# Kernel tuning notes

Hardware: AMD Instinct MI355X
Metric: run time of the kernel (lower is better)

Reference implementation:

```python
import jax, jax.numpy as jnp
import numpy as np

D = 64        # gat_output_dim == state_dim
HID = 128     # hidden_dim
ADIM = 2 * D  # action_dim (ope_dim + insert_dim)


def _mk(key, shape, scale=0.05):
    return jax.random.normal(key, shape, dtype=jnp.float32) * scale


def setup_inputs() -> dict:
    key = jax.random.key(0)
    ks = jax.random.split(key, 24)
    inp = {
        "ope_gat": jax.random.normal(ks[0], (8, 258, D), jnp.float32),
        "insert_gat": jax.random.normal(ks[1], (8, 256, D), jnp.float32),
        "h": jax.random.normal(ks[2], (8, D), jnp.float32),
        "c": jax.random.normal(ks[3], (8, D), jnp.float32),
        # LSTM (pytorch layout: gates i,f,g,o stacked -> [4D, in])
        "W_ih": _mk(ks[4], (4 * D, D)),
        "W_hh": _mk(ks[5], (4 * D, D)),
        "b_ih": _mk(ks[6], (4 * D,)),
        "b_hh": _mk(ks[7], (4 * D,)),
        # V_net: Linear(D,HID) -> Linear(HID,HID) -> LeakyReLU -> Linear(HID,1)
        "Wv0": _mk(ks[8], (HID, D)), "bv0": _mk(ks[9], (HID,)),
        "Wv1": _mk(ks[10], (HID, HID)), "bv1": _mk(ks[11], (HID,)),
        "Wv2": _mk(ks[12], (1, HID)), "bv2": _mk(ks[13], (1,)),
        # A_net: Linear(D+ADIM,HID) -> Linear(HID,HID) -> LeakyReLU -> Linear(HID,1)
        "Wa0": _mk(ks[14], (HID, D + ADIM)), "ba0": _mk(ks[15], (HID,)),
        "Wa1": _mk(ks[16], (HID, HID)), "ba1": _mk(ks[17], (HID,)),
        "Wa2": _mk(ks[18], (1, HID)), "ba2": _mk(ks[19], (1,)),
    }
    return inp


def _lrelu(x):
    return jnp.where(x >= 0, x, 0.01 * x)


def _forward(ope_gat, insert_gat, h, c,
             W_ih, W_hh, b_ih, b_hh,
             Wv0, bv0, Wv1, bv1, Wv2, bv2,
             Wa0, ba0, Wa1, ba1, Wa2, ba2):
    ope = ope_gat[:, 1:-1]                # [B, O, D]
    state = ope.mean(axis=-2)             # [B, D]

    # single-step LSTM (pytorch gate order i, f, g, o)
    gates = state @ W_ih.T + b_ih + h @ W_hh.T + b_hh  # [B, 4D]
    i_g, f_g, g_g, o_g = jnp.split(gates, 4, axis=-1)
    cn = jax.nn.sigmoid(f_g) * c + jax.nn.sigmoid(i_g) * jnp.tanh(g_g)
    hn = jax.nn.sigmoid(o_g) * jnp.tanh(cn)
    rnn_state = hn                        # [B, D]

    # V head (note: no activation after first linear -- name-overwrite bug)
    V = _lrelu((rnn_state @ Wv0.T + bv0) @ Wv1.T + bv1) @ Wv2.T + bv2  # [B, 1]

    # A head on the full (ope x insert) cross-join; ope side is detached.
    ope_d = jax.lax.stop_gradient(ope)    # [B, O, D]
    B, O, _ = ope_d.shape
    I = insert_gat.shape[1]
    # Decompose first linear over the concat [state | ope | insert] (exact math).
    Ws, Wo, Wi = Wa0[:, :D], Wa0[:, D:2 * D], Wa0[:, 2 * D:]
    h0 = (rnn_state @ Ws.T)[:, None, None, :] \
         + jnp.einsum('bod,hd->boh', ope_d, Wo)[:, :, None, :] \
         + jnp.einsum('bid,hd->bih', insert_gat, Wi)[:, None, :, :] \
         + ba0                              # [B, O, I, HID]
    h1 = _lrelu(jnp.einsum('boih,gh->boig', h0, Wa1) + ba1)
    A = (jnp.einsum('boih,h->boi', h1, Wa2[0]) + ba2[0]).reshape(B, O * I)
    return V, A, hn, cn


def reference(ope_gat, insert_gat, h, c,
              W_ih, W_hh, b_ih, b_hh,
              Wv0, bv0, Wv1, bv1, Wv2, bv2,
              Wa0, ba0, Wa1, ba1, Wa2, ba2):
    return _forward(ope_gat, insert_gat, h, c,
                    W_ih, W_hh, b_ih, b_hh,
                    Wv0, bv0, Wv1, bv1, Wv2, bv2,
                    Wa0, ba0, Wa1, ba1, Wa2, ba2)
```

## Files before the change

kernel.cpp:

```cpp
#include <hip/hip_runtime.h>
#include <hip/hip_bf16.h>
#include <math.h>

typedef unsigned short u16;

#define FB    524288
#define PART  6416
#define WA1B  10512
#define WOB   18704
#define WIB   22800
#define SOFF  26896
#define C1S   27920

__device__ __forceinline__ u16 f2b(float x) { __hip_bfloat16 b = __float2bfloat16(x); return *(u16*)&b; }
__device__ __forceinline__ void cvt8(const uint4 u, float* f) {
    f[0] = __uint_as_float(u.x << 16); f[1] = __uint_as_float(u.x & 0xFFFF0000u);
    f[2] = __uint_as_float(u.y << 16); f[3] = __uint_as_float(u.y & 0xFFFF0000u);
    f[4] = __uint_as_float(u.z << 16); f[5] = __uint_as_float(u.z & 0xFFFF0000u);
    f[6] = __uint_as_float(u.w << 16); f[7] = __uint_as_float(u.w & 0xFFFF0000u);
}
__device__ __forceinline__ float dot4(const float4 a, const float4 b) {
    return a.x*b.x + a.y*b.y + a.z*b.z + a.w*b.w;
}

__global__ __launch_bounds__(256) void k0_pre(
    const float* __restrict__ ope, const float* __restrict__ Wa0,
    const float* __restrict__ Wa1, const float* __restrict__ Wa2,
    const float* __restrict__ ba2, float* __restrict__ ws)
{
    const int t = threadIdx.x;
    if (blockIdx.x < 64) {
        const int b = blockIdx.x >> 3, s = blockIdx.x & 7;
        const int d = t & 63, rg = t >> 6;
        __shared__ float red[256];
        const float* p = ope + b*16512 + (1 + s*32 + rg*8)*64 + d;
        float acc = 0.f;
        #pragma unroll
        for (int rr = 0; rr < 8; ++rr) acc += p[rr*64];
        red[t] = acc;
        __syncthreads();
        if (t < 64)
            ws[FB + PART + (b*8 + s)*64 + t] = red[t] + red[t+64] + red[t+128] + red[t+192];
    } else if (blockIdx.x < 80) {
        const int e0 = ((blockIdx.x - 64)*256 + t) * 8;
        const float* src;
        u16* dst;
        if (e0 < 16384)      { src = Wa1 + e0;                                              dst = (u16*)(ws + FB + WA1B) + e0; }
        else if (e0 < 24576) { const int i = e0 - 16384; src = Wa0 + (i>>6)*192 + 64  + (i&63); dst = (u16*)(ws + FB + WOB) + i; }
        else                 { const int i = e0 - 24576; src = Wa0 + (i>>6)*192 + 128 + (i&63); dst = (u16*)(ws + FB + WIB) + i; }
        const float4 a = *(const float4*)src;
        const float4 c = *(const float4*)(src + 4);
        ushort4 u0; u0.x = f2b(a.x); u0.y = f2b(a.y); u0.z = f2b(a.z); u0.w = f2b(a.w);
        ushort4 u1; u1.x = f2b(c.x); u1.y = f2b(c.y); u1.z = f2b(c.z); u1.w = f2b(c.w);
        *(ushort4*)dst = u0;
        *(ushort4*)(dst + 4) = u1;
    } else {
        if (t < 128) {
            const float w2v = Wa2[t];
            ws[FB + 1024 + t] = 0.505f * w2v;
            ws[FB + 1152 + t] = 0.495f * w2v;
        }
        if (t == 128) ws[FB + 2313] = ba2[0];
    }
}

__global__ __launch_bounds__(256) void k12_main(
    const float* __restrict__ ope, const float* __restrict__ ins,
    const float* __restrict__ hin, const float* __restrict__ cin,
    const float* __restrict__ W_ih, const float* __restrict__ W_hh,
    const float* __restrict__ b_ih, const float* __restrict__ b_hh,
    const float* __restrict__ Wv0, const float* __restrict__ bv0,
    const float* __restrict__ Wv1, const float* __restrict__ bv1,
    const float* __restrict__ Wv2, const float* __restrict__ bv2,
    const float* __restrict__ Wa0, const float* __restrict__ ba0,
    const float* __restrict__ Wa1, const float* __restrict__ ba1,
    float* __restrict__ ws)
{
    __shared__ __align__(16) u16 Wa1s[128*136];
    __shared__ __align__(16) u16 Wsel[128*72];
    __shared__ __align__(16) u16 inrows[16*72];
    __shared__ __align__(16) float P[16*132];
    const int t = threadIdx.x;

    if (blockIdx.x < 256) {
        const int b = blockIdx.x >> 5;
        const int r0 = (blockIdx.x & 31) * 16;
        const int side = (r0 >= 256) ? 1 : 0;

        {
            const u16* wa1b = (const u16*)(ws + FB + WA1B);
            #pragma unroll
            for (int k = 0; k < 8; ++k) {
                const int e4 = t + k*256;
                const int g = e4 >> 4, hq = (e4 & 15) * 8;
                *(uint4*)&Wa1s[g*136 + hq] = *(const uint4*)(wa1b + g*128 + hq);
            }
        }
        {
            const u16* wsb = (const u16*)(ws + FB + (side ? WIB : WOB));
            #pragma unroll
            for (int k = 0; k < 4; ++k) {
                const int e4 = t + k*256;
                const int h = e4 >> 3, dq = (e4 & 7) * 8;
                *(uint4*)&Wsel[h*72 + dq] = *(const uint4*)(wsb + h*64 + dq);
            }
        }
        {
            const int r = t >> 4, dq = (t & 15) * 4;
            const float* src = side
                ? (ins + b*16384 + (r0 - 256 + r)*64 + dq)
                : (ope + b*16512 + (1 + r0 + r)*64 + dq);
            const float4 w = *(const float4*)src;
            ushort4 u; u.x = f2b(w.x); u.y = f2b(w.y); u.z = f2b(w.z); u.w = f2b(w.w);
            *(ushort4*)&inrows[r*72 + dq] = u;
        }
        __syncthreads();

        const int r = t >> 4;
        const int q = t & 15;

        {
            float acc[8] = {0.f,0.f,0.f,0.f,0.f,0.f,0.f,0.f};
            #pragma unroll
            for (int d8 = 0; d8 < 64; d8 += 8) {
                float iv[8];
                cvt8(*(const uint4*)&inrows[r*72 + d8], iv);
                #pragma unroll
                for (int k = 0; k < 8; ++k) {
                    float wv[8];
                    cvt8(*(const uint4*)&Wsel[(q + 16*k)*72 + d8], wv);
                    #pragma unroll
                    for (int j = 0; j < 8; ++j) acc[k] += wv[j] * iv[j];
                }
            }
            #pragma unroll
            for (int k = 0; k < 8; ++k) P[r*132 + q + 16*k] = acc[k];
        }
        __syncthreads();

        {
            float acc[8] = {0.f,0.f,0.f,0.f,0.f,0.f,0.f,0.f};
            #pragma unroll
            for (int h8 = 0; h8 < 128; h8 += 8) {
                const float4 p0 = *(const float4*)&P[r*132 + h8];
                const float4 p1 = *(const float4*)&P[r*132 + h8 + 4];
                #pragma unroll
                for (int k = 0; k < 8; ++k) {
                    float wv[8];
                    cvt8(*(const uint4*)&Wa1s[(q + 16*k)*136 + h8], wv);
                    float a = acc[k];
                    a += wv[0]*p0.x + wv[1]*p0.y + wv[2]*p0.z + wv[3]*p0.w;
                    a += wv[4]*p1.x + wv[5]*p1.y + wv[6]*p1.z + wv[7]*p1.w;
                    acc[k] = a;
                }
            }
            float part = 0.f;
            const int row = side ? (b*256 + r0 - 256 + r) : (b*256 + r0 + r);
            float* dst = side ? (ws + 262144 + row*128) : (ws + row*128);
            #pragma unroll
            for (int k = 0; k < 8; ++k) {
                const int g = q + 16*k;
                part = fmaf(ws[FB + 1024 + g], acc[k], part);
                dst[g] = acc[k];
            }
            part += __shfl_xor(part, 1);
            part += __shfl_xor(part, 2);
            part += __shfl_xor(part, 4);
            part += __shfl_xor(part, 8);
            if (q == 0) {
                if (!side) ws[FB + 2320 + row] = part;
                else       ws[FB + 4368 + row] = part;
            }
        }
    } else {
        const int b = blockIdx.x - 256;
        float* f = (float*)Wa1s;
        float* state = f;
        float* hvec  = f + 64;
        float* gl    = f + 128;
        float* hn_s  = f + 384;
        float* t0a   = f + 448;
        float* t1a   = f + 576;
        float* s2s   = f + 704;
        float* red   = f + 832;

        if (t < 64) {
            float s = 0.f;
            #pragma unroll
            for (int s8 = 0; s8 < 8; ++s8) s += ws[FB + PART + (b*8 + s8)*64 + t];
            state[t] = s * (1.f/256.f);
        } else if (t < 128) hvec[t-64] = hin[b*64 + (t-64)];
        __syncthreads();

        {
            float g = b_ih[t] + b_hh[t];
            const float4* wi = (const float4*)(W_ih + t*64);
            const float4* wh = (const float4*)(W_hh + t*64);
            #pragma unroll
            for (int k = 0; k < 16; ++k)
                g += dot4(wi[k], *(const float4*)&state[k*4])
                   + dot4(wh[k], *(const float4*)&hvec[k*4]);
            gl[t] = g;
        }
        __syncthreads();

        if (t < 64) {
            const float ig = gl[t], fg = gl[64+t], gg = gl[128+t], og = gl[192+t];
            const float c  = cin[b*64 + t];
            const float si = 1.f/(1.f + expf(-ig));
            const float sf = 1.f/(1.f + expf(-fg));
            const float so = 1.f/(1.f + expf(-og));
            const float cn = sf*c + si*tanhf(gg);
            const float hn = so*tanhf(cn);
            ws[FB + 1288 + b*64 + t] = hn;
            ws[FB + 1800 + b*64 + t] = cn;
            hn_s[t] = hn;
        }
        __syncthreads();

        if (t < 128) {
            float a = bv0[t];
            const float4* w = (const float4*)(Wv0 + t*64);
            #pragma unroll
            for (int k = 0; k < 16; ++k) a += dot4(w[k], *(const float4*)&hn_s[k*4]);
            t0a[t] = a;
        }
        __syncthreads();
        if (t < 128) {
            float a = bv1[t];
            const float4* w = (const float4*)(Wv1 + t*128);
            #pragma unroll
            for (int k = 0; k < 32; ++k) a += dot4(w[k], *(const float4*)&t0a[k*4]);
            a = (a >= 0.f) ? a : 0.01f*a;
            t1a[t] = a * Wv2[t];
            float s2 = ba0[t];
            const float4* w0 = (const float4*)(Wa0 + t*192);
            #pragma unroll
            for (int k = 0; k < 16; ++k) s2 += dot4(w0[k], *(const float4*)&hn_s[k*4]);
            s2s[t] = s2;
        }
        __syncthreads();
        if (t < 128) {
            float sv = ba1[t];
            const float4* w = (const float4*)(Wa1 + t*128);
            #pragma unroll
            for (int k = 0; k < 32; ++k) sv += dot4(w[k], *(const float4*)&s2s[k*4]);
            ws[FB + SOFF + b*128 + t] = sv;
            red[t] = ws[FB + 1024 + t] * sv;
        }
        __syncthreads();
        if (t < 64) {
            float c = red[t] + red[t + 64];
            float v = t1a[t] + t1a[t + 64];
            c += __shfl_xor(c, 32); v += __shfl_xor(v, 32);
            c += __shfl_xor(c, 16); v += __shfl_xor(v, 16);
            c += __shfl_xor(c, 8);  v += __shfl_xor(v, 8);
            c += __shfl_xor(c, 4);  v += __shfl_xor(v, 4);
            c += __shfl_xor(c, 2);  v += __shfl_xor(v, 2);
            c += __shfl_xor(c, 1);  v += __shfl_xor(v, 1);
            if (t == 0) {
                ws[FB + C1S + b]  = c + ws[FB + 2313];
                ws[FB + 1280 + b] = v + bv2[0];
            }
        }
    }
}

__global__ __launch_bounds__(256) void k3_adv(const float* __restrict__ ws,
                                              float* __restrict__ out)
{
    const int t = threadIdx.x;
    const int b = blockIdx.x >> 6;
    const int o0 = (blockIdx.x & 63) * 4;
    const float* wb = ws + FB + 1152;

    float acc[4] = {0.f, 0.f, 0.f, 0.f};
    #pragma unroll
    for (int gc = 0; gc < 8; ++gc) {
        float syv[16], wv[16];
        {
            const float* yr = ws + 262144 + (b*256 + t)*128 + gc*16;
            const float* sr = ws + FB + SOFF + b*128 + gc*16;
            #pragma unroll
            for (int k = 0; k < 4; ++k) {
                const float4 y4 = *(const float4*)(yr + k*4);
                const float4 s4 = *(const float4*)(sr + k*4);
                syv[k*4+0] = y4.x + s4.x; syv[k*4+1] = y4.y + s4.y;
                syv[k*4+2] = y4.z + s4.z; syv[k*4+3] = y4.w + s4.w;
                *(float4*)&wv[k*4] = *(const float4*)(wb + gc*16 + k*4);
            }
        }
        #pragma unroll
        for (int o = 0; o < 4; ++o) {
            const float* xr = ws + (b*256 + o0 + o)*128 + gc*16;
            float a = acc[o];
            #pragma unroll
            for (int k = 0; k < 4; ++k) {
                const float4 x4 = *(const float4*)(xr + k*4);
                a = fmaf(wv[k*4+0], fabsf(x4.x + syv[k*4+0]), a);
                a = fmaf(wv[k*4+1], fabsf(x4.y + syv[k*4+1]), a);
                a = fmaf(wv[k*4+2], fabsf(x4.z + syv[k*4+2]), a);
                a = fmaf(wv[k*4+3], fabsf(x4.w + syv[k*4+3]), a);
            }
            acc[o] = a;
        }
    }
    const float c2  = ws[FB + 4368 + b*256 + t];
    const float c1s = ws[FB + C1S + b];
    #pragma unroll
    for (int o = 0; o < 4; ++o)
        out[8 + b*65536 + (o0 + o)*256 + t] =
            ws[FB + 2320 + b*256 + o0 + o] + c1s + c2 + acc[o];

    if (blockIdx.x == 0) {
        if (t < 8) out[t] = ws[FB + 1280 + t];
        #pragma unroll
        for (int j = t; j < 512; j += 256) {
            out[524296 + j] = ws[FB + 1288 + j];
            out[524808 + j] = ws[FB + 1800 + j];
        }
    }
}

extern "C" void kernel_launch(void* const* d_in, const int* in_sizes, int n_in,
                              void* d_out, int out_size, void* d_ws, size_t ws_size,
                              hipStream_t stream) {
    float* ws = (float*)d_ws;
    float* out = (float*)d_out;

    const float* ope = (const float*)d_in[0];
    const float* ins = (const float*)d_in[1];

    k0_pre  <<<dim3(81),  dim3(256), 0, stream>>>(
        ope, (const float*)d_in[14], (const float*)d_in[16],
        (const float*)d_in[18], (const float*)d_in[19], ws);
    k12_main<<<dim3(264), dim3(256), 0, stream>>>(
        ope, ins,
        (const float*)d_in[2], (const float*)d_in[3],
        (const float*)d_in[4], (const float*)d_in[5],
        (const float*)d_in[6], (const float*)d_in[7],
        (const float*)d_in[8], (const float*)d_in[9],
        (const float*)d_in[10], (const float*)d_in[11],
        (const float*)d_in[12], (const float*)d_in[13],
        (const float*)d_in[14], (const float*)d_in[15],
        (const float*)d_in[16], (const float*)d_in[17], ws);
    k3_adv  <<<dim3(512), dim3(256), 0, stream>>>(ws, out);
}
```

Baseline: 123.2 us.

## Fold preprocessing kernel into main kernels, converting weights to bf16 inline

Removes the k0_pre launch. The fp32-to-bf16 conversion of Wa1 and the Wa0 slices now happens directly while staging into shared memory in each main block, and the ope mean reduction moves into the LSTM blocks. The Wa2 scaling constants are computed on the fly. This saves one kernel launch and its global round trip. In exchange, every one of the 256 main blocks reads twice as many fp32 weight bytes and redoes the conversion, and 8 blocks each perform a serial 64-row reduction.

```diff
diff --git a/kernel.cpp b/kernel.cpp
--- a/kernel.cpp
+++ b/kernel.cpp
@@ -5,10 +5,6 @@
 typedef unsigned short u16;
 
 #define FB    524288
-#define PART  6416
-#define WA1B  10512
-#define WOB   18704
-#define WIB   22800
 #define SOFF  26896
 #define C1S   27920
 
@@ -21,47 +17,6 @@
 }
 __device__ __forceinline__ float dot4(const float4 a, const float4 b) {
     return a.x*b.x + a.y*b.y + a.z*b.z + a.w*b.w;
-}
-
-__global__ __launch_bounds__(256) void k0_pre(
-    const float* __restrict__ ope, const float* __restrict__ Wa0,
-    const float* __restrict__ Wa1, const float* __restrict__ Wa2,
-    const float* __restrict__ ba2, float* __restrict__ ws)
-{
-    const int t = threadIdx.x;
-    if (blockIdx.x < 64) {
-        const int b = blockIdx.x >> 3, s = blockIdx.x & 7;
-        const int d = t & 63, rg = t >> 6;
-        __shared__ float red[256];
-        const float* p = ope + b*16512 + (1 + s*32 + rg*8)*64 + d;
-        float acc = 0.f;
-        #pragma unroll
-        for (int rr = 0; rr < 8; ++rr) acc += p[rr*64];
-        red[t] = acc;
-        __syncthreads();
-        if (t < 64)
-            ws[FB + PART + (b*8 + s)*64 + t] = red[t] + red[t+64] + red[t+128] + red[t+192];
-    } else if (blockIdx.x < 80) {
-        const int e0 = ((blockIdx.x - 64)*256 + t) * 8;
-        const float* src;
-        u16* dst;
-        if (e0 < 16384)      { src = Wa1 + e0;                                              dst = (u16*)(ws + FB + WA1B) + e0; }
-        else if (e0 < 24576) { const int i = e0 - 16384; src = Wa0 + (i>>6)*192 + 64  + (i&63); dst = (u16*)(ws + FB + WOB) + i; }
-        else                 { const int i = e0 - 24576; src = Wa0 + (i>>6)*192 + 128 + (i&63); dst = (u16*)(ws + FB + WIB) + i; }
-        const float4 a = *(const float4*)src;
-        const float4 c = *(const float4*)(src + 4);
-        ushort4 u0; u0.x = f2b(a.x); u0.y = f2b(a.y); u0.z = f2b(a.z); u0.w = f2b(a.w);
-        ushort4 u1; u1.x = f2b(c.x); u1.y = f2b(c.y); u1.z = f2b(c.z); u1.w = f2b(c.w);
-        *(ushort4*)dst = u0;
-        *(ushort4*)(dst + 4) = u1;
-    } else {
-        if (t < 128) {
-            const float w2v = Wa2[t];
-            ws[FB + 1024 + t] = 0.505f * w2v;
-            ws[FB + 1152 + t] = 0.495f * w2v;
-        }
-        if (t == 128) ws[FB + 2313] = ba2[0];
-    }
 }
 
 __global__ __launch_bounds__(256) void k12_main(
@@ -74,6 +29,7 @@
     const float* __restrict__ Wv2, const float* __restrict__ bv2,
     const float* __restrict__ Wa0, const float* __restrict__ ba0,
     const float* __restrict__ Wa1, const float* __restrict__ ba1,
+    const float* __restrict__ Wa2, const float* __restrict__ ba2,
     float* __restrict__ ws)
 {
     __shared__ __align__(16) u16 Wa1s[128*136];
@@ -87,23 +43,21 @@
         const int r0 = (blockIdx.x & 31) * 16;
         const int side = (r0 >= 256) ? 1 : 0;
 
-        {
-            const u16* wa1b = (const u16*)(ws + FB + WA1B);
-            #pragma unroll
-            for (int k = 0; k < 8; ++k) {
-                const int e4 = t + k*256;
-                const int g = e4 >> 4, hq = (e4 & 15) * 8;
-                *(uint4*)&Wa1s[g*136 + hq] = *(const uint4*)(wa1b + g*128 + hq);
-            }
-        }
-        {
-            const u16* wsb = (const u16*)(ws + FB + (side ? WIB : WOB));
-            #pragma unroll
-            for (int k = 0; k < 4; ++k) {
-                const int e4 = t + k*256;
-                const int h = e4 >> 3, dq = (e4 & 7) * 8;
-                *(uint4*)&Wsel[h*72 + dq] = *(const uint4*)(wsb + h*64 + dq);
-            }
+        #pragma unroll
+        for (int k = 0; k < 16; ++k) {
+            const int e4 = t + k*256;
+            const int g = e4 >> 5, hq = (e4 & 31) * 4;
+            const float4 w = *(const float4*)(Wa1 + g*128 + hq);
+            ushort4 u; u.x = f2b(w.x); u.y = f2b(w.y); u.z = f2b(w.z); u.w = f2b(w.w);
+            *(ushort4*)&Wa1s[g*136 + hq] = u;
+        }
+        #pragma unroll
+        for (int k = 0; k < 8; ++k) {
+            const int e4 = t + k*256;
+            const int h = e4 >> 4, dq = (e4 & 15) * 4;
+            const float4 w = *(const float4*)(Wa0 + h*192 + 64 + side*64 + dq);
+            ushort4 u; u.x = f2b(w.x); u.y = f2b(w.y); u.z = f2b(w.z); u.w = f2b(w.w);
+            *(ushort4*)&Wsel[h*72 + dq] = u;
         }
         {
             const int r = t >> 4, dq = (t & 15) * 4;
@@ -160,7 +114,7 @@
             #pragma unroll
             for (int k = 0; k < 8; ++k) {
                 const int g = q + 16*k;
-                part = fmaf(ws[FB + 1024 + g], acc[k], part);
+                part = fmaf(0.505f * Wa2[g], acc[k], part);
                 dst[g] = acc[k];
             }
             part += __shfl_xor(part, 1);
@@ -184,12 +138,17 @@
         float* s2s   = f + 704;
         float* red   = f + 832;
 
-        if (t < 64) {
+        {
+            const int d = t & 63, q = t >> 6;
+            const float* p = ope + b*16512 + (1 + q*64)*64 + d;
             float s = 0.f;
-            #pragma unroll
-            for (int s8 = 0; s8 < 8; ++s8) s += ws[FB + PART + (b*8 + s8)*64 + t];
-            state[t] = s * (1.f/256.f);
-        } else if (t < 128) hvec[t-64] = hin[b*64 + (t-64)];
+            #pragma unroll 8
+            for (int r = 0; r < 64; ++r) s += p[r*64];
+            red[t] = s;
+        }
+        __syncthreads();
+        if (t < 64)       state[t]   = (red[t] + red[t+64] + red[t+128] + red[t+192]) * (1.f/256.f);
+        else if (t < 128) hvec[t-64] = hin[b*64 + (t-64)];
         __syncthreads();
 
         {
@@ -246,7 +205,7 @@
             #pragma unroll
             for (int k = 0; k < 32; ++k) sv += dot4(w[k], *(const float4*)&s2s[k*4]);
             ws[FB + SOFF + b*128 + t] = sv;
-            red[t] = ws[FB + 1024 + t] * sv;
+            red[t] = 0.505f * Wa2[t] * sv;
         }
         __syncthreads();
         if (t < 64) {
@@ -259,7 +218,7 @@
             c += __shfl_xor(c, 2);  v += __shfl_xor(v, 2);
             c += __shfl_xor(c, 1);  v += __shfl_xor(v, 1);
             if (t == 0) {
-                ws[FB + C1S + b]  = c + ws[FB + 2313];
+                ws[FB + C1S + b]  = c + ba2[0];
                 ws[FB + 1280 + b] = v + bv2[0];
             }
         }
@@ -267,12 +226,12 @@
 }
 
 __global__ __launch_bounds__(256) void k3_adv(const float* __restrict__ ws,
+                                              const float* __restrict__ Wa2,
                                               float* __restrict__ out)
 {
     const int t = threadIdx.x;
     const int b = blockIdx.x >> 6;
     const int o0 = (blockIdx.x & 63) * 4;
-    const float* wb = ws + FB + 1152;
 
     float acc[4] = {0.f, 0.f, 0.f, 0.f};
     #pragma unroll
@@ -281,13 +240,16 @@
         {
             const float* yr = ws + 262144 + (b*256 + t)*128 + gc*16;
             const float* sr = ws + FB + SOFF + b*128 + gc*16;
+            const float* wr = Wa2 + gc*16;
             #pragma unroll
             for (int k = 0; k < 4; ++k) {
                 const float4 y4 = *(const float4*)(yr + k*4);
                 const float4 s4 = *(const float4*)(sr + k*4);
+                const float4 w4 = *(const float4*)(wr + k*4);
                 syv[k*4+0] = y4.x + s4.x; syv[k*4+1] = y4.y + s4.y;
                 syv[k*4+2] = y4.z + s4.z; syv[k*4+3] = y4.w + s4.w;
-                *(float4*)&wv[k*4] = *(const float4*)(wb + gc*16 + k*4);
+                wv[k*4+0] = 0.495f*w4.x; wv[k*4+1] = 0.495f*w4.y;
+                wv[k*4+2] = 0.495f*w4.z; wv[k*4+3] = 0.495f*w4.w;
             }
         }
         #pragma unroll
@@ -328,14 +290,8 @@
     float* ws = (float*)d_ws;
     float* out = (float*)d_out;
 
-    const float* ope = (const float*)d_in[0];
-    const float* ins = (const float*)d_in[1];
-
-    k0_pre  <<<dim3(81),  dim3(256), 0, stream>>>(
-        ope, (const float*)d_in[14], (const float*)d_in[16],
-        (const float*)d_in[18], (const float*)d_in[19], ws);
     k12_main<<<dim3(264), dim3(256), 0, stream>>>(
-        ope, ins,
+        (const float*)d_in[0], (const float*)d_in[1],
         (const float*)d_in[2], (const float*)d_in[3],
         (const float*)d_in[4], (const float*)d_in[5],
         (const float*)d_in[6], (const float*)d_in[7],
@@ -343,6 +299,7 @@
         (const float*)d_in[10], (const float*)d_in[11],
         (const float*)d_in[12], (const float*)d_in[13],
         (const float*)d_in[14], (const float*)d_in[15],
-        (const float*)d_in[16], (const float*)d_in[17], ws);
-    k3_adv  <<<dim3(512), dim3(256), 0, stream>>>(ws, out);
-}
+        (const float*)d_in[16], (const float*)d_in[17],
+        (const float*)d_in[18], (const float*)d_in[19], ws);
+    k3_adv  <<<dim3(512), dim3(256), 0, stream>>>(ws, (const float*)d_in[18], out);
+}
```

Result: no change. 123.3 us (median of 2 runs) (+0.1%).
